# Kernel optimization log

Measured on AMD Instinct MI355X. Metric: run time of the kernel, lower is better.

The kernel has to match this reference:

```python
import jax, jax.numpy as jnp
import numpy as np


def setup_inputs() -> dict:
    key = jax.random.key(0)
    ks = jax.random.split(key, 8)
    b, m, e, d = 8, 4096, 2048, 128
    features = jax.random.normal(ks[0], (b, m, d), dtype=jnp.float32)
    # sparse-ish binary incidence matrix (nodes x hyperedges)
    inc_mat = (jax.random.uniform(ks[1], (b, m, e)) < 0.02).astype(jnp.float32)
    s = 1.0 / np.sqrt(d)
    return {
        "features": features,
        "inc_mat": inc_mat,
        "vc_Wa": jax.random.uniform(ks[2], (d, d), minval=-s, maxval=s),
        "vc_Wp": jax.random.uniform(ks[3], (d, d), minval=-s, maxval=s),
        "vc_alpha": jnp.float32(0.5),
        "ec_Wa": jax.random.uniform(ks[4], (d, d), minval=-s, maxval=s),
        "ec_Wp": jax.random.uniform(ks[5], (d, d), minval=-s, maxval=s),
        "ec_alpha": jnp.float32(0.5),
        "n_layers": 3,
    }


def _vertex_conv(feat, inc, Wa, Wp, alpha, prev=None):
    # feat: [b,m,d], inc: [b,m,e]
    att = feat @ Wa.T                                   # [b,m,d]
    e_att = jnp.einsum('bme,bmd->bed', inc, att)        # inc^T @ att
    attw = jax.nn.softmax(e_att, axis=1)                # softmax over edges
    agg = jnp.einsum('bme,bmd->bed', inc, feat)         # collapsed bmed outer-product + contract
    ef = (agg * attw) @ Wp.T                            # [b,e,d]
    if prev is not None:
        ef = alpha * prev + (1.0 - alpha) * ef
    return ef


def _edge_conv(inc, edge_feats, Wa, Wp, alpha, prev=None):
    # NOTE: original EdgeConv computes softmax attention_weights but never uses them (dead code).
    w = jnp.einsum('bed,bme->bmd', edge_feats, inc)     # inc @ edge_feats
    nf = w @ Wp.T                                       # [b,m,d]
    if prev is not None:
        nf = alpha * prev + (1.0 - alpha) * nf
    return nf


def reference(features, inc_mat, vc_Wa, vc_Wp, vc_alpha, ec_Wa, ec_Wp, ec_alpha, n_layers):
    edge_feats = _vertex_conv(features, inc_mat, vc_Wa, vc_Wp, vc_alpha)
    node_feats = _edge_conv(inc_mat, edge_feats, ec_Wa, ec_Wp, ec_alpha)
    for _ in range(1, n_layers):
        edge_feats = _vertex_conv(features, inc_mat, vc_Wa, vc_Wp, vc_alpha, prev=edge_feats)
        node_feats = _edge_conv(inc_mat, edge_feats, ec_Wa, ec_Wp, ec_alpha, prev=node_feats)
    return node_feats, edge_feats
```

## Files before the change

kernel.cpp:

```cpp
#include <hip/hip_runtime.h>

#define BB 8
#define MM 4096
#define EE 2048
#define DD 128

typedef _Float16 f16x8 __attribute__((ext_vector_type(8)));
typedef float    f32x4 __attribute__((ext_vector_type(4)));

__global__ __launch_bounds__(256) void transpose_to16(const float* __restrict__ src,
                                                      _Float16* __restrict__ dst,
                                                      int R, int C)
{
    __shared__ alignas(16) float tile[64 * 67];
    const int tilesC = C >> 6;
    const int r0 = (blockIdx.x / tilesC) << 6;
    const int c0 = (blockIdx.x % tilesC) << 6;
    const float* s = src + (size_t)blockIdx.y * R * C;
    _Float16*   d = dst + (size_t)blockIdx.y * R * C;
    const int t = threadIdx.x;
    #pragma unroll
    for (int i = 0; i < 4; i++){
        int idx = t + 256 * i;
        int r = idx >> 4, c4 = idx & 15;
        float4 v = *(const float4*)(s + (size_t)(r0 + r) * C + c0 + c4 * 4);
        tile[(c4 * 4 + 0) * 67 + r] = v.x;
        tile[(c4 * 4 + 1) * 67 + r] = v.y;
        tile[(c4 * 4 + 2) * 67 + r] = v.z;
        tile[(c4 * 4 + 3) * 67 + r] = v.w;
    }
    __syncthreads();
    #pragma unroll
    for (int i = 0; i < 2; i++){
        int idx = t + 256 * i;
        int row = idx >> 3, rb = idx & 7;
        f16x8 h;
        #pragma unroll
        for (int j = 0; j < 8; j++) h[j] = (_Float16)tile[row * 67 + rb * 8 + j];
        *(f16x8*)(d + (size_t)(c0 + row) * R + r0 + rb * 8) = h;
    }
}

__global__ __launch_bounds__(256, 1) void fused_gemm1(const float* __restrict__ inc,
                                                      const _Float16* __restrict__ featT,
                                                      unsigned long long* __restrict__ bitsX,
                                                      float* __restrict__ p)
{
    __shared__ alignas(16) char smem[36864];

    const int x = blockIdx.x;
    const int b = blockIdx.y;
    const int z = blockIdx.z;
    const int t = threadIdx.x, lane = t & 63, w = t >> 6;
    const int fr = lane & 15, q = lane >> 4, q8 = q * 8;

    const int e0 = x * 256;
    const int ew0 = e0 + w * 64;
    const _Float16* dp = featT + (size_t)b * 128 * MM;
    const float* ip = inc + (size_t)b * MM * EE + ew0 + lane;
    unsigned long long* bxp = bitsX + ((size_t)b * 32 + (x * 4 + w)) * MM;

    f32x4 acc[4][8] = {};
    uint4 rd[4];
    float val[64];

    auto loadg = [&](int k0){
        #pragma unroll
        for (int i = 0; i < 4; i++){
            int idx = t + 256 * i;
            int dd = idx >> 3, kb = idx & 7;
            rd[i] = *(const uint4*)(dp + (size_t)dd * MM + k0 + kb * 8);
        }
        const float* rp = ip + (size_t)k0 * EE;
        #pragma unroll
        for (int j = 0; j < 64; j++) val[j] = rp[(size_t)j * EE];
    };
    auto stage = [&](int buf, int k0){
        _Float16* lD = (_Float16*)(smem + buf * 16384);
        unsigned long long* lBits = (unsigned long long*)(smem + 32768 + buf * 2048);
        #pragma unroll
        for (int i = 0; i < 4; i++){
            int idx = t + 256 * i;
            int dd = idx >> 3, kb = idx & 7;
            *(uint4*)&lD[dd * 64 + ((kb ^ (dd & 7)) * 8)] = rd[i];
        }
        unsigned long long wbits = 0;
        #pragma unroll
        for (int j = 0; j < 64; j++){
            unsigned long long bal = __ballot(val[j] != 0.0f);
            wbits = (lane == j) ? bal : wbits;
        }
        bxp[k0 + lane] = wbits;
        unsigned long long wT = 0;
        #pragma unroll
        for (int ei = 0; ei < 64; ei++){
            unsigned long long bal = __ballot((wbits >> ei) & 1ull);
            wT = (lane == ei) ? bal : wT;
        }
        lBits[w * 64 + lane] = wT;
    };
    auto compute = [&](int buf){
        const _Float16* lD = (const _Float16*)(smem + buf * 16384);
        const uint2* lBits = (const uint2*)(smem + 32768 + buf * 2048);
        uint2 bw[4];
        f16x8 af[4][2];
        #pragma unroll
        for (int s = 0; s < 4; s++) bw[s] = lBits[w * 64 + s * 16 + fr];
        #pragma unroll
        for (int s = 0; s < 4; s++)
            #pragma unroll
            for (int h = 0; h < 2; h++){
                unsigned word = h ? bw[s].y : bw[s].x;
                unsigned byte = (word >> q8) & 0xFFu;
                #pragma unroll
                for (int j = 0; j < 8; j++)
                    af[s][h][j] = ((byte >> j) & 1u) ? (_Float16)1.0f : (_Float16)0.0f;
            }
        #pragma unroll
        for (int h = 0; h < 2; h++)
            #pragma unroll
            for (int c = 0; c < 8; c++){
                int drow = c * 16 + fr;
                f16x8 bf = *(const f16x8*)&lD[drow * 64 + (((h * 4 + q) ^ (drow & 7)) * 8)];
                #pragma unroll
                for (int s = 0; s < 4; s++)
                    acc[s][c] = __builtin_amdgcn_mfma_f32_16x16x32_f16(af[s][h], bf, acc[s][c], 0, 0, 0);
            }
    };

    const int kbase = z * 1024;
    loadg(kbase); stage(0, kbase); __syncthreads();
    for (int c = 0; c < 16; c++){
        if (c + 1 < 16) loadg(kbase + (c + 1) * 64);
        compute(c & 1);
        if (c + 1 < 16) stage((c + 1) & 1, kbase + (c + 1) * 64);
        __syncthreads();
    }

    float* sT = (float*)smem;
    float* op = p + (size_t)z * 2097152 + ((size_t)b * EE + e0) * 128;
    for (int ph = 0; ph < 4; ph++){
        __syncthreads();
        if (w == ph){
            #pragma unroll
            for (int s = 0; s < 4; s++)
                #pragma unroll
                for (int c = 0; c < 8; c++)
                    #pragma unroll
                    for (int reg = 0; reg < 4; reg++)
                        sT[(s * 16 + q * 4 + reg) * 132 + c * 16 + fr] = acc[s][c][reg];
        }
        __syncthreads();
        #pragma unroll
        for (int i = 0; i < 8; i++){
            int idx = t + 256 * i;
            int lrow = idx >> 5, c4 = idx & 31;
            float4 v = *(const float4*)&sT[lrow * 132 + c4 * 4];
            *(float4*)(op + (size_t)(ph * 64 + lrow) * 128 + c4 * 4) = v;
        }
    }
}

__global__ __launch_bounds__(256) void bitgemm2_fused(const unsigned long long* __restrict__ bitsX,
                                                      const _Float16* __restrict__ PT,
                                                      const _Float16* __restrict__ Wc16,
                                                      float* __restrict__ node)
{
    __shared__ alignas(16) char smem[66560];
    const int b = blockIdx.y;
    const int m0 = blockIdx.x * 64;
    const unsigned long long* bxp = bitsX + (size_t)b * 32 * MM;
    const _Float16* dp = PT + (size_t)b * 128 * EE;
    float* op = node + ((size_t)b * MM + m0) * 128;

    const int t = threadIdx.x, lane = t & 63, w = t >> 6;
    const int fr = lane & 15, q = lane >> 4, q8 = q * 8;

    _Float16* lWc = (_Float16*)(smem + 33792);
    #pragma unroll
    for (int i = 0; i < 8; i++){
        int idx = t + 256 * i;
        int n = idx >> 4, kb = idx & 15;
        *(uint4*)&lWc[n * 128 + ((kb ^ (n & 7)) * 8)] =
            *(const uint4*)(Wc16 + (size_t)n * 128 + kb * 8);
    }

    f32x4 acc[8] = {};
    uint4 rd[4];
    unsigned long long rb;

    auto loadg = [&](int kg){
        #pragma unroll
        for (int i = 0; i < 4; i++){
            int idx = t + 256 * i;
            int dd = idx >> 3, kb = idx & 7;
            rd[i] = *(const uint4*)(dp + (size_t)dd * EE + kg + kb * 8);
        }
        if (t < 64) rb = bxp[(size_t)(kg >> 6) * MM + m0 + t];
    };
    auto stage = [&](int buf){
        _Float16* lD = (_Float16*)(smem + buf * 16384);
        unsigned long long* lB = (unsigned long long*)(smem + 32768 + buf * 512);
        #pragma unroll
        for (int i = 0; i < 4; i++){
            int idx = t + 256 * i;
            int dd = idx >> 3, kb = idx & 7;
            *(uint4*)&lD[dd * 64 + ((kb ^ (dd & 7)) * 8)] = rd[i];
        }
        if (t < 64) lB[t] = rb;
    };
    auto compute = [&](int buf){
        const _Float16* lD = (const _Float16*)(smem + buf * 16384);
        const uint2* lB = (const uint2*)(smem + 32768 + buf * 512);
        uint2 bw = lB[w * 16 + fr];
        #pragma unroll
        for (int h = 0; h < 2; h++){
            unsigned word = h ? bw.y : bw.x;
            unsigned byte = (word >> q8) & 0xFFu;
            f16x8 af;
            #pragma unroll
            for (int j = 0; j < 8; j++)
                af[j] = ((byte >> j) & 1u) ? (_Float16)1.0f : (_Float16)0.0f;
            #pragma unroll
            for (int c = 0; c < 8; c++){
                int drow = c * 16 + fr;
                f16x8 bf = *(const f16x8*)&lD[drow * 64 + (((h * 4 + q) ^ (drow & 7)) * 8)];
                acc[c] = __builtin_amdgcn_mfma_f32_16x16x32_f16(af, bf, acc[c], 0, 0, 0);
            }
        }
    };

    loadg(0); stage(0); __syncthreads();
    for (int c = 0; c < 32; c++){
        if (c + 1 < 32) loadg((c + 1) * 64);
        compute(c & 1);
        if (c + 1 < 32) stage((c + 1) & 1);
        __syncthreads();
    }

    _Float16* sQ = (_Float16*)smem;
    #pragma unroll
    for (int c = 0; c < 8; c++){
        #pragma unroll
        for (int reg = 0; reg < 4; reg++){
            int row = w * 16 + q * 4 + reg;
            int col = c * 16 + fr;
            sQ[row * 128 + (((col >> 3) ^ (row & 7)) * 8) + (col & 7)] = (_Float16)acc[c][reg];
        }
    }
    f32x4 acc2[8] = {};
    #pragma unroll
    for (int kk = 0; kk < 4; kk++){
        int arow = w * 16 + fr;
        f16x8 a2 = *(const f16x8*)&sQ[arow * 128 + (((kk * 4 + q) ^ (arow & 7)) * 8)];
        #pragma unroll
        for (int c = 0; c < 8; c++){
            int n = c * 16 + fr;
            f16x8 b2 = *(const f16x8*)&lWc[n * 128 + (((kk * 4 + q) ^ (n & 7)) * 8)];
            acc2[c] = __builtin_amdgcn_mfma_f32_16x16x32_f16(a2, b2, acc2[c], 0, 0, 0);
        }
    }
    __syncthreads();
    float* sD = (float*)smem;
    #pragma unroll
    for (int c = 0; c < 8; c++)
        #pragma unroll
        for (int reg = 0; reg < 4; reg++)
            sD[(w * 16 + q * 4 + reg) * 132 + c * 16 + fr] = acc2[c][reg];
    __syncthreads();
    #pragma unroll
    for (int i = 0; i < 8; i++){
        int idx = t + 256 * i;
        int lrow = idx >> 5, c4 = idx & 31;
        float4 v = *(const float4*)&sD[lrow * 132 + c4 * 4];
        *(float4*)(op + (size_t)lrow * 128 + c4 * 4) = v;
    }
}

__global__ __launch_bounds__(256) void rowmm_sum4(const float* __restrict__ p,
                                                  const float* __restrict__ W,
                                                  float* aggOut,
                                                  float* __restrict__ C)
{
    __shared__ alignas(16) float lA[32][132];
    __shared__ alignas(16) float lW[64][140];
    const int t = threadIdx.x;
    const int row0 = blockIdx.x * 32;
    const float4* P4 = (const float4*)p;
    const float4* W4 = (const float4*)W;
    float4* A4 = (float4*)aggOut;
    const size_t SS = 2097152 / 4;

    #pragma unroll
    for (int i = 0; i < 4; i++){
        int idx = t + 256 * i;
        int r = idx >> 5, k4 = idx & 31;
        size_t gi = (size_t)(row0 + r) * 32 + k4;
        float4 a = P4[gi], b = P4[gi + SS], c = P4[gi + 2 * SS], d = P4[gi + 3 * SS];
        float4 s = make_float4(a.x + b.x + c.x + d.x, a.y + b.y + c.y + d.y,
                               a.z + b.z + c.z + d.z, a.w + b.w + c.w + d.w);
        *(float4*)&lA[r][k4 * 4] = s;
        A4[gi] = s;
    }
    const int qq = t >> 5, cc = t & 31;

    #pragma unroll
    for (int ph = 0; ph < 2; ph++){
        __syncthreads();
        #pragma unroll
        for (int i = 0; i < 8; i++){
            int idx = t + 256 * i;
            int c = idx >> 5, k4 = idx & 31;
            *(float4*)&lW[c][k4 * 4] = W4[(size_t)(ph * 64 + c) * 32 + k4];
        }
        __syncthreads();
        float s[4][2] = {};
        for (int k4 = 0; k4 < 32; k4++){
            float4 w0 = *(const float4*)&lW[cc][k4 * 4];
            float4 w1 = *(const float4*)&lW[cc + 32][k4 * 4];
            #pragma unroll
            for (int j = 0; j < 4; j++){
                float4 a = *(const float4*)&lA[qq + 8 * j][k4 * 4];
                s[j][0] += a.x * w0.x + a.y * w0.y + a.z * w0.z + a.w * w0.w;
                s[j][1] += a.x * w1.x + a.y * w1.y + a.z * w1.z + a.w * w1.w;
            }
        }
        #pragma unroll
        for (int j = 0; j < 4; j++){
            size_t ro = (size_t)(row0 + qq + 8 * j) * DD + ph * 64;
            C[ro + cc]      = s[j][0];
            C[ro + cc + 32] = s[j][1];
        }
    }
}

__global__ __launch_bounds__(256) void rowmm(const float* A,
                                             const float* __restrict__ W,
                                             float* C)
{
    __shared__ alignas(16) float lA[32][132];
    __shared__ alignas(16) float lW[64][140];
    const int t = threadIdx.x;
    const int row0 = blockIdx.x * 32;
    const float4* A4 = (const float4*)A;
    const float4* W4 = (const float4*)W;

    #pragma unroll
    for (int i = 0; i < 4; i++){
        int idx = t + 256 * i;
        int r = idx >> 5, k4 = idx & 31;
        *(float4*)&lA[r][k4 * 4] = A4[(size_t)(row0 + r) * 32 + k4];
    }
    const int qq = t >> 5, cc = t & 31;

    #pragma unroll
    for (int ph = 0; ph < 2; ph++){
        __syncthreads();
        #pragma unroll
        for (int i = 0; i < 8; i++){
            int idx = t + 256 * i;
            int c = idx >> 5, k4 = idx & 31;
            *(float4*)&lW[c][k4 * 4] = W4[(size_t)(ph * 64 + c) * 32 + k4];
        }
        __syncthreads();
        float s[4][2] = {};
        for (int k4 = 0; k4 < 32; k4++){
            float4 w0 = *(const float4*)&lW[cc][k4 * 4];
            float4 w1 = *(const float4*)&lW[cc + 32][k4 * 4];
            #pragma unroll
            for (int j = 0; j < 4; j++){
                float4 a = *(const float4*)&lA[qq + 8 * j][k4 * 4];
                s[j][0] += a.x * w0.x + a.y * w0.y + a.z * w0.z + a.w * w0.w;
                s[j][1] += a.x * w1.x + a.y * w1.y + a.z * w1.z + a.w * w1.w;
            }
        }
        #pragma unroll
        for (int j = 0; j < 4; j++){
            size_t ro = (size_t)(row0 + qq + 8 * j) * DD + ph * 64;
            C[ro + cc]      = s[j][0];
            C[ro + cc + 32] = s[j][1];
        }
    }
}

__global__ __launch_bounds__(256) void wc_mm16(const float* __restrict__ eWp,
                                               const float* __restrict__ vWp,
                                               _Float16* __restrict__ Wc16)
{
    int i = blockIdx.x * 2 + (threadIdx.x >> 7);
    int j = threadIdx.x & 127;
    float acc = 0.f;
    for (int k = 0; k < 128; k++)
        acc += eWp[i * 128 + k] * vWp[k * 128 + j];
    Wc16[i * 128 + j] = (_Float16)acc;
}

__global__ __launch_bounds__(256) void sm_part(const float* __restrict__ eatt,
                                               float* __restrict__ part)
{
    const int b = blockIdx.x, slab = blockIdx.y;
    const int t = threadIdx.x;
    const int dl = t & 127, eh = t >> 7;
    const size_t base = (size_t)b * EE * DD + dl;
    const int e0 = slab * 256;
    float m = -1e30f;
    for (int s = 0; s < 128; s++)
        m = fmaxf(m, eatt[base + (size_t)(e0 + eh + 2 * s) * DD]);
    float l = 0.f;
    for (int s = 0; s < 128; s++)
        l += __expf(eatt[base + (size_t)(e0 + eh + 2 * s) * DD] - m);
    __shared__ float red[2][128][2];
    red[eh][dl][0] = m; red[eh][dl][1] = l;
    __syncthreads();
    if (t < 128){
        float m0 = red[0][t][0], l0 = red[0][t][1];
        float m1 = red[1][t][0], l1 = red[1][t][1];
        float M = fmaxf(m0, m1);
        float L = l0 * __expf(m0 - M) + l1 * __expf(m1 - M);
        float* pp = part + ((size_t)(b * 8 + slab) * DD + t) * 2;
        pp[0] = M; pp[1] = L;
    }
}

__global__ __launch_bounds__(256) void sm_apply(float* __restrict__ eatt,
                                                const float* __restrict__ agg,
                                                const float* __restrict__ part)
{
    const int b = blockIdx.x, sl = blockIdx.y;
    const int t = threadIdx.x;
    __shared__ float mv[128], iv[128];
    if (t < 128){
        float mbuf[8], lbuf[8];
        float M = -1e30f;
        #pragma unroll
        for (int s = 0; s < 8; s++){
            const float* pp = part + ((size_t)(b * 8 + s) * DD + t) * 2;
            mbuf[s] = pp[0]; lbuf[s] = pp[1];
            M = fmaxf(M, mbuf[s]);
        }
        float L = 0.f;
        #pragma unroll
        for (int s = 0; s < 8; s++) L += lbuf[s] * __expf(mbuf[s] - M);
        mv[t] = M; iv[t] = 1.f / L;
    }
    __syncthreads();
    const int dl = t & 127, eh = t >> 7;
    const size_t base = (size_t)b * EE * DD + dl;
    const int e0 = sl * 128;
    for (int s = 0; s < 64; s++){
        size_t ix = base + (size_t)(e0 + eh + 2 * s) * DD;
        eatt[ix] = agg[ix] * __expf(eatt[ix] - mv[dl]) * iv[dl];
    }
}

extern "C" void kernel_launch(void* const* d_in, const int* in_sizes, int n_in,
                              void* d_out, int out_size, void* d_ws, size_t ws_size,
                              hipStream_t stream)
{
    const float* feat = (const float*)d_in[0];
    const float* inc  = (const float*)d_in[1];
    const float* vWa  = (const float*)d_in[2];
    const float* vWp  = (const float*)d_in[3];
    const float* eWp  = (const float*)d_in[6];

    float* node_out = (float*)d_out;
    float* edge_out = node_out + (size_t)BB * MM * DD;

    char* w = (char*)d_ws;
    unsigned long long* bitsX = (unsigned long long*)w;
    float* pk  = (float*)(w + ((size_t)8 << 20));
    float* agg = pk;
    _Float16* PT = (_Float16*)(w + ((size_t)16 << 20));
    _Float16* Wc16 = (_Float16*)(w + ((size_t)40 << 20));

    _Float16* featT = (_Float16*)node_out;
    float* eattP = node_out + 2097152;
    float* part  = edge_out;

    dim3 blk(256);

    transpose_to16<<<dim3((MM / 64) * (DD / 64), BB), blk, 0, stream>>>(feat, featT, MM, DD);
    wc_mm16<<<dim3(64), blk, 0, stream>>>(eWp, vWp, Wc16);
    fused_gemm1<<<dim3(EE / 256, BB, 4), blk, 0, stream>>>(inc, featT, bitsX, pk);
    rowmm_sum4<<<dim3(BB * EE / 32), blk, 0, stream>>>(pk, vWa, agg, eattP);
    sm_part <<<dim3(BB, 8),  blk, 0, stream>>>(eattP, part);
    sm_apply<<<dim3(BB, 16), blk, 0, stream>>>(eattP, agg, part);
    rowmm<<<dim3(BB * EE / 32), blk, 0, stream>>>(eattP, vWp, edge_out);
    transpose_to16<<<dim3((EE / 64) * (DD / 64), BB), blk, 0, stream>>>(eattP, PT, EE, DD);
    bitgemm2_fused<<<dim3(MM / 64, BB), blk, 0, stream>>>(bitsX, PT, Wc16, node_out);
}
```

Before: 564.9 us.

## Specialize waves into loader/ballot and feature roles, halve split-K in gemm1

The first fused GEMM now uses 128-edge tiles with a 2-way K split instead of 256-edge tiles with a 4-way split. Within each block, two waves read the incidence matrix and build the bitmasks while the other two load the fp16 features into LDS. All four waves then run the MFMA compute on 32 edge rows each. This halves the partial-sum buffer traffic and the reduction work in the follow-up rowmm_sum kernel, and keeps the same total block count. The trade-off is fewer waves feeding the strided incidence reads, which may lower memory-level parallelism on the dominant 268MB read, plus more loop iterations per block.

After: 569.7 us. No clear change (+0.8%).

```diff
diff --git a/kernel.cpp b/kernel.cpp
--- a/kernel.cpp
+++ b/kernel.cpp
@@ -46,7 +46,7 @@
                                                       unsigned long long* __restrict__ bitsX,
                                                       float* __restrict__ p)
 {
-    __shared__ alignas(16) char smem[36864];
+    __shared__ alignas(16) char smem[34816];
 
     const int x = blockIdx.x;
     const int b = blockIdx.y;
@@ -54,101 +54,107 @@
     const int t = threadIdx.x, lane = t & 63, w = t >> 6;
     const int fr = lane & 15, q = lane >> 4, q8 = q * 8;
 
-    const int e0 = x * 256;
-    const int ew0 = e0 + w * 64;
+    const int e0 = x * 128;
     const _Float16* dp = featT + (size_t)b * 128 * MM;
-    const float* ip = inc + (size_t)b * MM * EE + ew0 + lane;
-    unsigned long long* bxp = bitsX + ((size_t)b * 32 + (x * 4 + w)) * MM;
-
-    f32x4 acc[4][8] = {};
-    uint4 rd[4];
+    const float* ip = inc + (size_t)b * MM * EE + e0 + (w & 1) * 64 + lane;
+    unsigned long long* bxp = bitsX + ((size_t)b * 32 + (x * 2 + (w & 1))) * MM;
+
+    f32x4 acc[2][8] = {};
     float val[64];
+    uint4 rd[8];
 
     auto loadg = [&](int k0){
-        #pragma unroll
-        for (int i = 0; i < 4; i++){
-            int idx = t + 256 * i;
-            int dd = idx >> 3, kb = idx & 7;
-            rd[i] = *(const uint4*)(dp + (size_t)dd * MM + k0 + kb * 8);
-        }
-        const float* rp = ip + (size_t)k0 * EE;
-        #pragma unroll
-        for (int j = 0; j < 64; j++) val[j] = rp[(size_t)j * EE];
+        if (w < 2){
+            const float* rp = ip + (size_t)k0 * EE;
+            #pragma unroll
+            for (int j = 0; j < 64; j++) val[j] = rp[(size_t)j * EE];
+        } else {
+            #pragma unroll
+            for (int i = 0; i < 8; i++){
+                int vid = (w - 2) * 64 + lane + 128 * i;
+                int dd = vid >> 3, kb = vid & 7;
+                rd[i] = *(const uint4*)(dp + (size_t)dd * MM + k0 + kb * 8);
+            }
+        }
     };
     auto stage = [&](int buf, int k0){
-        _Float16* lD = (_Float16*)(smem + buf * 16384);
-        unsigned long long* lBits = (unsigned long long*)(smem + 32768 + buf * 2048);
-        #pragma unroll
-        for (int i = 0; i < 4; i++){
-            int idx = t + 256 * i;
-            int dd = idx >> 3, kb = idx & 7;
-            *(uint4*)&lD[dd * 64 + ((kb ^ (dd & 7)) * 8)] = rd[i];
-        }
-        unsigned long long wbits = 0;
-        #pragma unroll
-        for (int j = 0; j < 64; j++){
-            unsigned long long bal = __ballot(val[j] != 0.0f);
-            wbits = (lane == j) ? bal : wbits;
-        }
-        bxp[k0 + lane] = wbits;
-        unsigned long long wT = 0;
-        #pragma unroll
-        for (int ei = 0; ei < 64; ei++){
-            unsigned long long bal = __ballot((wbits >> ei) & 1ull);
-            wT = (lane == ei) ? bal : wT;
-        }
-        lBits[w * 64 + lane] = wT;
+        if (w < 2){
+            unsigned long long wbits = 0;
+            #pragma unroll
+            for (int j = 0; j < 64; j++){
+                unsigned long long bal = __ballot(val[j] != 0.0f);
+                wbits = (lane == j) ? bal : wbits;
+            }
+            bxp[k0 + lane] = wbits;
+            unsigned long long wT = 0;
+            #pragma unroll
+            for (int ei = 0; ei < 64; ei++){
+                unsigned long long bal = __ballot((wbits >> ei) & 1ull);
+                wT = (lane == ei) ? bal : wT;
+            }
+            unsigned long long* lBits = (unsigned long long*)(smem + 32768 + buf * 1024);
+            lBits[(w & 1) * 64 + lane] = wT;
+        } else {
+            _Float16* lD = (_Float16*)(smem + buf * 16384);
+            #pragma unroll
+            for (int i = 0; i < 8; i++){
+                int vid = (w - 2) * 64 + lane + 128 * i;
+                int dd = vid >> 3, kb = vid & 7;
+                *(uint4*)&lD[dd * 64 + ((kb ^ (dd & 7)) * 8)] = rd[i];
+            }
+        }
     };
     auto compute = [&](int buf){
         const _Float16* lD = (const _Float16*)(smem + buf * 16384);
-        const uint2* lBits = (const uint2*)(smem + 32768 + buf * 2048);
-        uint2 bw[4];
-        f16x8 af[4][2];
-        #pragma unroll
-        for (int s = 0; s < 4; s++) bw[s] = lBits[w * 64 + s * 16 + fr];
-        #pragma unroll
-        for (int s = 0; s < 4; s++)
-            #pragma unroll
-            for (int h = 0; h < 2; h++){
-                unsigned word = h ? bw[s].y : bw[s].x;
+        const uint2* lB = (const uint2*)(smem + 32768 + buf * 1024);
+        uint2 bw[2];
+        #pragma unroll
+        for (int r = 0; r < 2; r++)
+            bw[r] = lB[w * 32 + r * 16 + fr];
+        #pragma unroll
+        for (int h = 0; h < 2; h++){
+            f16x8 af[2];
+            #pragma unroll
+            for (int r = 0; r < 2; r++){
+                unsigned word = h ? bw[r].y : bw[r].x;
                 unsigned byte = (word >> q8) & 0xFFu;
                 #pragma unroll
                 for (int j = 0; j < 8; j++)
-                    af[s][h][j] = ((byte >> j) & 1u) ? (_Float16)1.0f : (_Float16)0.0f;
-            }
-        #pragma unroll
-        for (int h = 0; h < 2; h++)
+                    af[r][j] = ((byte >> j) & 1u) ? (_Float16)1.0f : (_Float16)0.0f;
+            }
             #pragma unroll
             for (int c = 0; c < 8; c++){
                 int drow = c * 16 + fr;
                 f16x8 bf = *(const f16x8*)&lD[drow * 64 + (((h * 4 + q) ^ (drow & 7)) * 8)];
                 #pragma unroll
-                for (int s = 0; s < 4; s++)
-                    acc[s][c] = __builtin_amdgcn_mfma_f32_16x16x32_f16(af[s][h], bf, acc[s][c], 0, 0, 0);
-            }
-    };
-
-    const int kbase = z * 1024;
+                for (int r = 0; r < 2; r++)
+                    acc[r][c] = __builtin_amdgcn_mfma_f32_16x16x32_f16(af[r], bf, acc[r][c], 0, 0, 0);
+            }
+        }
+    };
+
+    const int kbase = z * 2048;
     loadg(kbase); stage(0, kbase); __syncthreads();
-    for (int c = 0; c < 16; c++){
-        if (c + 1 < 16) loadg(kbase + (c + 1) * 64);
+    for (int c = 0; c < 32; c++){
+        if (c + 1 < 32) loadg(kbase + (c + 1) * 64);
         compute(c & 1);
-        if (c + 1 < 16) stage((c + 1) & 1, kbase + (c + 1) * 64);
+        if (c + 1 < 32) stage((c + 1) & 1, kbase + (c + 1) * 64);
         __syncthreads();
     }
 
     float* sT = (float*)smem;
     float* op = p + (size_t)z * 2097152 + ((size_t)b * EE + e0) * 128;
-    for (int ph = 0; ph < 4; ph++){
-        __syncthreads();
-        if (w == ph){
-            #pragma unroll
-            for (int s = 0; s < 4; s++)
+    for (int ph = 0; ph < 2; ph++){
+        __syncthreads();
+        if ((w >> 1) == ph){
+            int rbase = (w & 1) * 32;
+            #pragma unroll
+            for (int r = 0; r < 2; r++)
                 #pragma unroll
                 for (int c = 0; c < 8; c++)
                     #pragma unroll
                     for (int reg = 0; reg < 4; reg++)
-                        sT[(s * 16 + q * 4 + reg) * 132 + c * 16 + fr] = acc[s][c][reg];
+                        sT[(rbase + r * 16 + q * 4 + reg) * 132 + c * 16 + fr] = acc[r][c][reg];
         }
         __syncthreads();
         #pragma unroll
@@ -277,7 +283,7 @@
     }
 }
 
-__global__ __launch_bounds__(256) void rowmm_sum4(const float* __restrict__ p,
+__global__ __launch_bounds__(256) void rowmm_sum2(const float* __restrict__ p,
                                                   const float* __restrict__ W,
                                                   float* aggOut,
                                                   float* __restrict__ C)
@@ -296,9 +302,8 @@
         int idx = t + 256 * i;
         int r = idx >> 5, k4 = idx & 31;
         size_t gi = (size_t)(row0 + r) * 32 + k4;
-        float4 a = P4[gi], b = P4[gi + SS], c = P4[gi + 2 * SS], d = P4[gi + 3 * SS];
-        float4 s = make_float4(a.x + b.x + c.x + d.x, a.y + b.y + c.y + d.y,
-                               a.z + b.z + c.z + d.z, a.w + b.w + c.w + d.w);
+        float4 a = P4[gi], b = P4[gi + SS];
+        float4 s = make_float4(a.x + b.x, a.y + b.y, a.z + b.z, a.w + b.w);
         *(float4*)&lA[r][k4 * 4] = s;
         A4[gi] = s;
     }
@@ -471,7 +476,7 @@
     float* pk  = (float*)(w + ((size_t)8 << 20));
     float* agg = pk;
     _Float16* PT = (_Float16*)(w + ((size_t)16 << 20));
-    _Float16* Wc16 = (_Float16*)(w + ((size_t)40 << 20));
+    _Float16* Wc16 = (_Float16*)(w + ((size_t)24 << 20));
 
     _Float16* featT = (_Float16*)node_out;
     float* eattP = node_out + 2097152;
@@ -481,8 +486,8 @@
 
     transpose_to16<<<dim3((MM / 64) * (DD / 64), BB), blk, 0, stream>>>(feat, featT, MM, DD);
     wc_mm16<<<dim3(64), blk, 0, stream>>>(eWp, vWp, Wc16);
-    fused_gemm1<<<dim3(EE / 256, BB, 4), blk, 0, stream>>>(inc, featT, bitsX, pk);
-    rowmm_sum4<<<dim3(BB * EE / 32), blk, 0, stream>>>(pk, vWa, agg, eattP);
+    fused_gemm1<<<dim3(EE / 128, BB, 2), blk, 0, stream>>>(inc, featT, bitsX, pk);
+    rowmm_sum2<<<dim3(BB * EE / 32), blk, 0, stream>>>(pk, vWa, agg, eattP);
     sm_part <<<dim3(BB, 8),  blk, 0, stream>>>(eattP, part);
     sm_apply<<<dim3(BB, 16), blk, 0, stream>>>(eattP, agg, part);
     rowmm<<<dim3(BB * EE / 32), blk, 0, stream>>>(eattP, vWp, edge_out);
```
